# Performance work log

Hardware: AMD Instinct MI355X
Metric: run time of the kernel (lower is better)

## Reference

```python
import jax, jax.numpy as jnp
import numpy as np

N_HEADS = 16
D_EMBED = 1024
HEAD_DIM = D_EMBED // N_HEADS


def setup_inputs() -> dict:
    key = jax.random.key(0)
    ks = jax.random.split(key, 9)
    s = 1.0 / np.sqrt(D_EMBED)
    def lin(kw, kb):
        W = jax.random.uniform(kw, (D_EMBED, D_EMBED), jnp.float32, -s, s)
        b = jax.random.uniform(kb, (D_EMBED,), jnp.float32, -s, s)
        return W, b
    q_w, q_b = lin(ks[0], ks[1])
    k_w, k_b = lin(ks[2], ks[3])
    v_w, v_b = lin(ks[4], ks[5])
    o_w, o_b = lin(ks[6], ks[7])
    x = jax.random.normal(ks[8], (4, 2048, D_EMBED), jnp.float32)
    return {"x": x, "q_w": q_w, "q_b": q_b, "k_w": k_w, "k_b": k_b,
            "v_w": v_w, "v_b": v_b, "o_w": o_w, "o_b": o_b}


def reference(x, q_w, q_b, k_w, k_b, v_w, v_b, o_w, o_b):
    B, S, _ = x.shape
    # projections; W stored as [in, out] so y = x @ W + b (matches nn.Linear math)
    def split_heads(y):
        return y.reshape(B, S, N_HEADS, HEAD_DIM).transpose(0, 2, 1, 3)  # [B,H,S,D]
    q = split_heads(x @ q_w + q_b)
    k = split_heads(x @ k_w + k_b)
    v = split_heads(x @ v_w + v_b)
    scale = 1.0 / np.sqrt(HEAD_DIM).astype(np.float32)
    scores = jnp.einsum('bhqd,bhkd->bhqk', q, k) * scale  # [B,H,S,S]
    weights = jax.nn.softmax(scores, axis=-1)
    attn = jnp.einsum('bhqk,bhkd->bhqd', weights, v)  # [B,H,S,D]
    attn = attn.transpose(0, 2, 1, 3).reshape(B, S, D_EMBED)
    return attn @ o_w + o_b
```

## Files before the change

### kernel.cpp

```cpp
#include <hip/hip_runtime.h>
#include <hip/hip_bf16.h>
#include <math.h>

typedef __attribute__((ext_vector_type(8))) short bf16x8;
typedef __attribute__((ext_vector_type(4))) float f32x4;

#define D_EMBED 1024
#define SEQ 2048
#define NH 16
#define HD 64
#define QSCALE 0.1803368801111204f

__device__ __forceinline__ short f2bf(float f) {
    union { float f; unsigned u; } v; v.f = f;
    return (short)((v.u + 0x7FFFu + ((v.u >> 16) & 1u)) >> 16);
}

__device__ __forceinline__ unsigned pk_bf16(float a, float b) {
#if __has_builtin(__builtin_amdgcn_cvt_pk_bf16_f32)
    typedef __attribute__((ext_vector_type(2))) __bf16 vbf2;
    union { vbf2 v; unsigned u; } c;
    c.v = __builtin_amdgcn_cvt_pk_bf16_f32(a, b);
    return c.u;
#else
    return (unsigned)(unsigned short)f2bf(a) | ((unsigned)(unsigned short)f2bf(b) << 16);
#endif
}

__device__ __forceinline__ float exp2f_(float x) {
#if __has_builtin(__builtin_amdgcn_exp2f)
    return __builtin_amdgcn_exp2f(x);
#else
    return __expf(x * 0.6931471805599453f);
#endif
}

typedef __attribute__((address_space(1))) const void gvoid_t;
typedef __attribute__((address_space(3))) void lvoid_t;
__device__ __forceinline__ void glds16(const void* g, void* l) {
    __builtin_amdgcn_global_load_lds((gvoid_t*)g, (lvoid_t*)l, 16, 0, 0);
}

__global__ __launch_bounds__(256) void xconv_kernel(const float* __restrict__ x,
                                                    short* __restrict__ xb)
{
    size_t i = ((size_t)blockIdx.x * 256 + threadIdx.x) * 8;
    float4 f0 = *(const float4*)(x + i);
    float4 f1 = *(const float4*)(x + i + 4);
    uint4 o;
    o.x = pk_bf16(f0.x, f0.y); o.y = pk_bf16(f0.z, f0.w);
    o.z = pk_bf16(f1.x, f1.y); o.w = pk_bf16(f1.z, f1.w);
    *(uint4*)(xb + i) = o;
}

__global__ __launch_bounds__(256) void wtrans_kernel(
    const float* __restrict__ w0, const float* __restrict__ w1,
    const float* __restrict__ w2, const float* __restrict__ w3,
    short* __restrict__ wt)
{
    __shared__ float tile[64][65];
    const float* W = (blockIdx.z == 0) ? w0 : (blockIdx.z == 1) ? w1
                   : (blockIdx.z == 2) ? w2 : w3;
    short* out = wt + (size_t)blockIdx.z * D_EMBED * D_EMBED;
    int k0 = blockIdx.x * 64, n0 = blockIdx.y * 64;
    #pragma unroll
    for (int i = 0; i < 16; i++) {
        int idx = threadIdx.x + i * 256; int r = idx >> 6, c = idx & 63;
        tile[r][c] = W[(size_t)(k0 + r) * D_EMBED + n0 + c];
    }
    __syncthreads();
    #pragma unroll
    for (int i = 0; i < 16; i++) {
        int idx = threadIdx.x + i * 256; int r = idx >> 6, c = idx & 63;
        out[(size_t)(n0 + r) * D_EMBED + k0 + c] = f2bf(tile[c][r]);
    }
}

__global__ __launch_bounds__(256) void gemm_qkv_kernel(
    const short* __restrict__ xb, const short* __restrict__ wt,
    const float* __restrict__ qb, const float* __restrict__ kb, const float* __restrict__ vb,
    short* __restrict__ qo, short* __restrict__ ko, short* __restrict__ vto)
{
    __shared__ __attribute__((aligned(16))) short As[128][32];
    __shared__ __attribute__((aligned(16))) short Bs[128][32];
    const int tid = threadIdx.x;
    const int lane = tid & 63, wv = tid >> 6;
    const int l16 = lane & 15, quad = lane >> 4;
    const int wm = (wv & 1) * 64, wn = (wv >> 1) * 64;
    const int m0 = blockIdx.y * 128, n0 = blockIdx.x * 128;

    const short* aptr0 = xb + (size_t)(m0 + (tid >> 2)) * D_EMBED + (tid & 3) * 8;
    const short* aptr1 = aptr0 + (size_t)64 * D_EMBED;
    const short* bptr0 = wt + (size_t)(n0 + (tid >> 2)) * D_EMBED + (tid & 3) * 8;
    const short* bptr1 = bptr0 + (size_t)64 * D_EMBED;
    char* aldsb = (char*)&As[0][0] + wv * 1024;
    char* bldsb = (char*)&Bs[0][0] + wv * 1024;

    f32x4 acc[4][4];
    #pragma unroll
    for (int a = 0; a < 4; a++)
        #pragma unroll
        for (int b = 0; b < 4; b++) acc[a][b] = (f32x4){0.f, 0.f, 0.f, 0.f};

    for (int k0 = 0; k0 < D_EMBED; k0 += 32) {
        __syncthreads();
        glds16(aptr0 + k0, aldsb);
        glds16(aptr1 + k0, aldsb + 4096);
        glds16(bptr0 + k0, bldsb);
        glds16(bptr1 + k0, bldsb + 4096);
        __syncthreads();
        bf16x8 af[4], bfr[4];
        #pragma unroll
        for (int mi = 0; mi < 4; mi++) af[mi]  = *(const bf16x8*)&As[wm + mi * 16 + l16][quad * 8];
        #pragma unroll
        for (int ni = 0; ni < 4; ni++) bfr[ni] = *(const bf16x8*)&Bs[wn + ni * 16 + l16][quad * 8];
        #pragma unroll
        for (int mi = 0; mi < 4; mi++)
            #pragma unroll
            for (int ni = 0; ni < 4; ni++)
                acc[mi][ni] = __builtin_amdgcn_mfma_f32_16x16x32_bf16(af[mi], bfr[ni], acc[mi][ni], 0, 0, 0);
    }

    const int zz = n0 >> 10;
    const int ncol0 = (n0 & 1023) + wn;
    const float* bias = (zz == 0) ? qb : (zz == 1) ? kb : vb;
    #pragma unroll
    for (int mi = 0; mi < 4; mi++)
        #pragma unroll
        for (int ni = 0; ni < 4; ni++)
            #pragma unroll
            for (int rg = 0; rg < 4; rg++) {
                int row = m0 + wm + mi * 16 + quad * 4 + rg;
                int col = ncol0 + ni * 16 + l16;
                float v = acc[mi][ni][rg] + bias[col];
                int b = row >> 11, s = row & 2047, h = col >> 6, d = col & 63;
                if (zz == 0)      qo[(((size_t)(b * NH + h)) * SEQ + s) * HD + d] = f2bf(v * QSCALE);
                else if (zz == 1) ko[(((size_t)(b * NH + h)) * SEQ + s) * HD + d] = f2bf(v);
                else              vto[(((size_t)(b * NH + h)) * HD + d) * SEQ + s] = f2bf(v);
            }
}

__global__ __launch_bounds__(256) void flash_kernel(
    const short* __restrict__ Q, const short* __restrict__ K,
    const short* __restrict__ Vt, short* __restrict__ attn)
{
    __shared__ __attribute__((aligned(16))) short Ks[64][64];
    __shared__ __attribute__((aligned(16))) short Vs[64][64];
    __shared__ __attribute__((aligned(16))) short Ps[4][64][72];
    const int bh = blockIdx.y, qt = blockIdx.x;
    const int tid = threadIdx.x, lane = tid & 63, wv = tid >> 6;
    const int l16 = lane & 15, quad = lane >> 4;
    const int sw = l16 & 7;

    bf16x8 qf[4][2];
    #pragma unroll
    for (int g = 0; g < 4; g++) {
        const short* qp = Q + ((size_t)bh * SEQ + qt * 256 + wv * 64 + g * 16 + l16) * HD;
        qf[g][0] = *(const bf16x8*)(qp + quad * 8);
        qf[g][1] = *(const bf16x8*)(qp + 32 + quad * 8);
    }

    const int sr = tid >> 3;
    const int scg = (tid & 7) ^ (sr & 7);
    const short* kp0 = K  + ((size_t)bh * SEQ + sr) * HD + scg * 8;
    const short* vp0 = Vt + ((size_t)bh * HD + sr) * SEQ + scg * 8;
    char* kldsb = (char*)&Ks[0][0] + wv * 1024;
    char* vldsb = (char*)&Vs[0][0] + wv * 1024;

    float lsum[4] = {0.f, 0.f, 0.f, 0.f};
    f32x4 oacc[4][4];
    #pragma unroll
    for (int g = 0; g < 4; g++)
        #pragma unroll
        for (int di = 0; di < 4; di++) oacc[g][di] = (f32x4){0.f, 0.f, 0.f, 0.f};

    for (int kt = 0; kt < SEQ; kt += 64) {
        __syncthreads();
        glds16(kp0 + (size_t)kt * HD, kldsb);
        glds16(kp0 + (size_t)(kt + 32) * HD, kldsb + 4096);
        glds16(vp0 + kt, vldsb);
        glds16(vp0 + (size_t)32 * SEQ + kt, vldsb + 4096);
        __syncthreads();

        bf16x8 kf[4][2];
        #pragma unroll
        for (int ni = 0; ni < 4; ni++) {
            kf[ni][0] = *(const bf16x8*)&Ks[ni * 16 + l16][((quad    ) ^ sw) * 8];
            kf[ni][1] = *(const bf16x8*)&Ks[ni * 16 + l16][((quad + 4) ^ sw) * 8];
        }

        #pragma unroll
        for (int g = 0; g < 4; g++) {
            f32x4 sacc[4];
            #pragma unroll
            for (int ni = 0; ni < 4; ni++) {
                sacc[ni] = (f32x4){0.f, 0.f, 0.f, 0.f};
                sacc[ni] = __builtin_amdgcn_mfma_f32_16x16x32_bf16(kf[ni][0], qf[g][0], sacc[ni], 0, 0, 0);
                sacc[ni] = __builtin_amdgcn_mfma_f32_16x16x32_bf16(kf[ni][1], qf[g][1], sacc[ni], 0, 0, 0);
            }
            short* prow = &Ps[wv][g * 16 + l16][0];
            float ps = 0.f;
            #pragma unroll
            for (int ni = 0; ni < 4; ni++) {
                float p0 = exp2f_(sacc[ni][0]);
                float p1 = exp2f_(sacc[ni][1]);
                float p2 = exp2f_(sacc[ni][2]);
                float p3 = exp2f_(sacc[ni][3]);
                ps += (p0 + p1) + (p2 + p3);
                uint2 pw; pw.x = pk_bf16(p0, p1); pw.y = pk_bf16(p2, p3);
                *(uint2*)(prow + ni * 16 + quad * 4) = pw;
            }
            lsum[g] += ps;
        }

        bf16x8 vf[4][2];
        #pragma unroll
        for (int di = 0; di < 4; di++) {
            vf[di][0] = *(const bf16x8*)&Vs[di * 16 + l16][((quad    ) ^ sw) * 8];
            vf[di][1] = *(const bf16x8*)&Vs[di * 16 + l16][((quad + 4) ^ sw) * 8];
        }
        #pragma unroll
        for (int g = 0; g < 4; g++) {
            const short* prow = &Ps[wv][g * 16 + l16][0];
            bf16x8 pf0 = *(const bf16x8*)(prow + quad * 8);
            bf16x8 pf1 = *(const bf16x8*)(prow + 32 + quad * 8);
            #pragma unroll
            for (int di = 0; di < 4; di++) {
                oacc[g][di] = __builtin_amdgcn_mfma_f32_16x16x32_bf16(pf0, vf[di][0], oacc[g][di], 0, 0, 0);
                oacc[g][di] = __builtin_amdgcn_mfma_f32_16x16x32_bf16(pf1, vf[di][1], oacc[g][di], 0, 0, 0);
            }
        }
    }

    const int b = bh >> 4, h = bh & 15;
    #pragma unroll
    for (int g = 0; g < 4; g++) {
        float l = lsum[g];
        l += __shfl_xor(l, 16);
        l += __shfl_xor(l, 32);
        float rl[4];
        #pragma unroll
        for (int rg = 0; rg < 4; rg++) rl[rg] = 1.0f / __shfl(l, quad * 4 + rg);
        #pragma unroll
        for (int di = 0; di < 4; di++)
            #pragma unroll
            for (int rg = 0; rg < 4; rg++) {
                int s = qt * 256 + wv * 64 + g * 16 + quad * 4 + rg;
                int col = h * HD + di * 16 + l16;
                attn[((size_t)b * SEQ + s) * D_EMBED + col] = f2bf(oacc[g][di][rg] * rl[rg]);
            }
    }
}

__global__ __launch_bounds__(256) void gemm_out_kernel(
    const short* __restrict__ attn, const short* __restrict__ wt_o,
    const float* __restrict__ ob, float* __restrict__ out)
{
    __shared__ __attribute__((aligned(16))) short As[128][32];
    __shared__ __attribute__((aligned(16))) short Bs[128][32];
    const int tid = threadIdx.x;
    const int lane = tid & 63, wv = tid >> 6;
    const int l16 = lane & 15, quad = lane >> 4;
    const int wm = (wv & 1) * 64, wn = (wv >> 1) * 64;
    const int m0 = blockIdx.y * 128, n0 = blockIdx.x * 128;

    const short* aptr0 = attn + (size_t)(m0 + (tid >> 2)) * D_EMBED + (tid & 3) * 8;
    const short* aptr1 = aptr0 + (size_t)64 * D_EMBED;
    const short* bptr0 = wt_o + (size_t)(n0 + (tid >> 2)) * D_EMBED + (tid & 3) * 8;
    const short* bptr1 = bptr0 + (size_t)64 * D_EMBED;
    char* aldsb = (char*)&As[0][0] + wv * 1024;
    char* bldsb = (char*)&Bs[0][0] + wv * 1024;

    f32x4 acc[4][4];
    #pragma unroll
    for (int a = 0; a < 4; a++)
        #pragma unroll
        for (int b = 0; b < 4; b++) acc[a][b] = (f32x4){0.f, 0.f, 0.f, 0.f};

    for (int k0 = 0; k0 < D_EMBED; k0 += 32) {
        __syncthreads();
        glds16(aptr0 + k0, aldsb);
        glds16(aptr1 + k0, aldsb + 4096);
        glds16(bptr0 + k0, bldsb);
        glds16(bptr1 + k0, bldsb + 4096);
        __syncthreads();
        bf16x8 af[4], bfr[4];
        #pragma unroll
        for (int mi = 0; mi < 4; mi++) af[mi]  = *(const bf16x8*)&As[wm + mi * 16 + l16][quad * 8];
        #pragma unroll
        for (int ni = 0; ni < 4; ni++) bfr[ni] = *(const bf16x8*)&Bs[wn + ni * 16 + l16][quad * 8];
        #pragma unroll
        for (int mi = 0; mi < 4; mi++)
            #pragma unroll
            for (int ni = 0; ni < 4; ni++)
                acc[mi][ni] = __builtin_amdgcn_mfma_f32_16x16x32_bf16(af[mi], bfr[ni], acc[mi][ni], 0, 0, 0);
    }

    #pragma unroll
    for (int mi = 0; mi < 4; mi++)
        #pragma unroll
        for (int ni = 0; ni < 4; ni++)
            #pragma unroll
            for (int rg = 0; rg < 4; rg++) {
                int row = m0 + wm + mi * 16 + quad * 4 + rg;
                int col = n0 + wn + ni * 16 + l16;
                out[(size_t)row * D_EMBED + col] = acc[mi][ni][rg] + ob[col];
            }
}

extern "C" void kernel_launch(void* const* d_in, const int* in_sizes, int n_in,
                              void* d_out, int out_size, void* d_ws, size_t ws_size,
                              hipStream_t stream) {
    const float* x  = (const float*)d_in[0];
    const float* qw = (const float*)d_in[1];
    const float* qb = (const float*)d_in[2];
    const float* kw = (const float*)d_in[3];
    const float* kb = (const float*)d_in[4];
    const float* vw = (const float*)d_in[5];
    const float* vb = (const float*)d_in[6];
    const float* ow = (const float*)d_in[7];
    const float* ob = (const float*)d_in[8];

    char* ws = (char*)d_ws;
    short* xb  = (short*)(ws);
    short* wt  = (short*)(ws + (size_t)(16 << 20));
    short* q   = (short*)(ws + (size_t)(24 << 20));
    short* k   = (short*)(ws + (size_t)(40 << 20));
    short* vt  = (short*)(ws + (size_t)(56 << 20));
    short* at  = xb;

    xconv_kernel<<<4096, 256, 0, stream>>>(x, xb);
    wtrans_kernel<<<dim3(16, 16, 4), 256, 0, stream>>>(qw, kw, vw, ow, wt);
    gemm_qkv_kernel<<<dim3(24, 64), 256, 0, stream>>>(xb, wt, qb, kb, vb, q, k, vt);
    flash_kernel<<<dim3(8, 64), 256, 0, stream>>>(q, k, vt, at);
    gemm_out_kernel<<<dim3(8, 64), 256, 0, stream>>>(at, wt + (size_t)3 * D_EMBED * D_EMBED, ob, (float*)d_out);
}
```

Before: 327.4 us.

## Merge prep kernels, stage V transpose via LDS, load K directly, shrink out-GEMM tile

Folds the x conversion and the weight transpose into one launch, saving a kernel launch. The V-projection epilogue now transposes through shared memory so V^T is written with coalesced 16-byte stores instead of scattered 2-byte stores. The flash kernel reads K fragments straight from global memory (relying on cache) instead of staging them in LDS, and moves one barrier later so the score computation can overlap the V load. The output GEMM uses 128x64 tiles, doubling its block count for better CU occupancy, at the cost of lower per-block data reuse.

Result: faster. 319.0 us (-2.6%).

```diff
diff --git a/kernel.cpp b/kernel.cpp
--- a/kernel.cpp
+++ b/kernel.cpp
@@ -41,38 +41,38 @@
     __builtin_amdgcn_global_load_lds((gvoid_t*)g, (lvoid_t*)l, 16, 0, 0);
 }
 
-__global__ __launch_bounds__(256) void xconv_kernel(const float* __restrict__ x,
-                                                    short* __restrict__ xb)
-{
-    size_t i = ((size_t)blockIdx.x * 256 + threadIdx.x) * 8;
-    float4 f0 = *(const float4*)(x + i);
-    float4 f1 = *(const float4*)(x + i + 4);
-    uint4 o;
-    o.x = pk_bf16(f0.x, f0.y); o.y = pk_bf16(f0.z, f0.w);
-    o.z = pk_bf16(f1.x, f1.y); o.w = pk_bf16(f1.z, f1.w);
-    *(uint4*)(xb + i) = o;
-}
-
-__global__ __launch_bounds__(256) void wtrans_kernel(
+__global__ __launch_bounds__(256) void prep_kernel(
+    const float* __restrict__ x,
     const float* __restrict__ w0, const float* __restrict__ w1,
     const float* __restrict__ w2, const float* __restrict__ w3,
-    short* __restrict__ wt)
+    short* __restrict__ wt, short* __restrict__ xb)
 {
     __shared__ float tile[64][65];
-    const float* W = (blockIdx.z == 0) ? w0 : (blockIdx.z == 1) ? w1
-                   : (blockIdx.z == 2) ? w2 : w3;
-    short* out = wt + (size_t)blockIdx.z * D_EMBED * D_EMBED;
-    int k0 = blockIdx.x * 64, n0 = blockIdx.y * 64;
-    #pragma unroll
-    for (int i = 0; i < 16; i++) {
-        int idx = threadIdx.x + i * 256; int r = idx >> 6, c = idx & 63;
-        tile[r][c] = W[(size_t)(k0 + r) * D_EMBED + n0 + c];
-    }
-    __syncthreads();
-    #pragma unroll
-    for (int i = 0; i < 16; i++) {
-        int idx = threadIdx.x + i * 256; int r = idx >> 6, c = idx & 63;
-        out[(size_t)(n0 + r) * D_EMBED + k0 + c] = f2bf(tile[c][r]);
+    const int bid = blockIdx.x;
+    if (bid < 1024) {
+        const int z = bid >> 8, rem = bid & 255;
+        const float* W = (z == 0) ? w0 : (z == 1) ? w1 : (z == 2) ? w2 : w3;
+        short* out = wt + (size_t)z * D_EMBED * D_EMBED;
+        int k0 = (rem & 15) * 64, n0 = (rem >> 4) * 64;
+        #pragma unroll
+        for (int i = 0; i < 16; i++) {
+            int idx = threadIdx.x + i * 256; int r = idx >> 6, c = idx & 63;
+            tile[r][c] = W[(size_t)(k0 + r) * D_EMBED + n0 + c];
+        }
+        __syncthreads();
+        #pragma unroll
+        for (int i = 0; i < 16; i++) {
+            int idx = threadIdx.x + i * 256; int r = idx >> 6, c = idx & 63;
+            out[(size_t)(n0 + r) * D_EMBED + k0 + c] = f2bf(tile[c][r]);
+        }
+    } else {
+        size_t i = ((size_t)(bid - 1024) * 256 + threadIdx.x) * 8;
+        float4 f0 = *(const float4*)(x + i);
+        float4 f1 = *(const float4*)(x + i + 4);
+        uint4 o;
+        o.x = pk_bf16(f0.x, f0.y); o.y = pk_bf16(f0.z, f0.w);
+        o.z = pk_bf16(f1.x, f1.y); o.w = pk_bf16(f1.z, f1.w);
+        *(uint4*)(xb + i) = o;
     }
 }
 
@@ -81,8 +81,10 @@
     const float* __restrict__ qb, const float* __restrict__ kb, const float* __restrict__ vb,
     short* __restrict__ qo, short* __restrict__ ko, short* __restrict__ vto)
 {
-    __shared__ __attribute__((aligned(16))) short As[128][32];
-    __shared__ __attribute__((aligned(16))) short Bs[128][32];
+    __shared__ __attribute__((aligned(16))) union ShQKV {
+        struct { short As[128][32]; short Bs[128][32]; } ab;
+        short Es[64][136];
+    } sh;
     const int tid = threadIdx.x;
     const int lane = tid & 63, wv = tid >> 6;
     const int l16 = lane & 15, quad = lane >> 4;
@@ -93,8 +95,8 @@
     const short* aptr1 = aptr0 + (size_t)64 * D_EMBED;
     const short* bptr0 = wt + (size_t)(n0 + (tid >> 2)) * D_EMBED + (tid & 3) * 8;
     const short* bptr1 = bptr0 + (size_t)64 * D_EMBED;
-    char* aldsb = (char*)&As[0][0] + wv * 1024;
-    char* bldsb = (char*)&Bs[0][0] + wv * 1024;
+    char* aldsb = (char*)&sh.ab.As[0][0] + wv * 1024;
+    char* bldsb = (char*)&sh.ab.Bs[0][0] + wv * 1024;
 
     f32x4 acc[4][4];
     #pragma unroll
@@ -111,9 +113,9 @@
         __syncthreads();
         bf16x8 af[4], bfr[4];
         #pragma unroll
-        for (int mi = 0; mi < 4; mi++) af[mi]  = *(const bf16x8*)&As[wm + mi * 16 + l16][quad * 8];
-        #pragma unroll
-        for (int ni = 0; ni < 4; ni++) bfr[ni] = *(const bf16x8*)&Bs[wn + ni * 16 + l16][quad * 8];
+        for (int mi = 0; mi < 4; mi++) af[mi]  = *(const bf16x8*)&sh.ab.As[wm + mi * 16 + l16][quad * 8];
+        #pragma unroll
+        for (int ni = 0; ni < 4; ni++) bfr[ni] = *(const bf16x8*)&sh.ab.Bs[wn + ni * 16 + l16][quad * 8];
         #pragma unroll
         for (int mi = 0; mi < 4; mi++)
             #pragma unroll
@@ -122,29 +124,60 @@
     }
 
     const int zz = n0 >> 10;
-    const int ncol0 = (n0 & 1023) + wn;
-    const float* bias = (zz == 0) ? qb : (zz == 1) ? kb : vb;
-    #pragma unroll
-    for (int mi = 0; mi < 4; mi++)
-        #pragma unroll
-        for (int ni = 0; ni < 4; ni++)
-            #pragma unroll
-            for (int rg = 0; rg < 4; rg++) {
-                int row = m0 + wm + mi * 16 + quad * 4 + rg;
-                int col = ncol0 + ni * 16 + l16;
-                float v = acc[mi][ni][rg] + bias[col];
-                int b = row >> 11, s = row & 2047, h = col >> 6, d = col & 63;
-                if (zz == 0)      qo[(((size_t)(b * NH + h)) * SEQ + s) * HD + d] = f2bf(v * QSCALE);
-                else if (zz == 1) ko[(((size_t)(b * NH + h)) * SEQ + s) * HD + d] = f2bf(v);
-                else              vto[(((size_t)(b * NH + h)) * HD + d) * SEQ + s] = f2bf(v);
-            }
+    if (zz == 2) {
+        const int b = m0 >> 11, st0 = m0 & 2047;
+        const int hbase = (n0 & 1023) >> 6;
+        #pragma unroll
+        for (int h2 = 0; h2 < 2; h2++) {
+            __syncthreads();
+            if ((wv >> 1) == h2) {
+                #pragma unroll
+                for (int mi = 0; mi < 4; mi++) {
+                    int sbase = (wv & 1) * 64 + mi * 16 + quad * 4;
+                    #pragma unroll
+                    for (int ni = 0; ni < 4; ni++) {
+                        int d = ni * 16 + l16;
+                        float bv = vb[(n0 & 1023) + h2 * 64 + d];
+                        uint2 pw;
+                        pw.x = pk_bf16(acc[mi][ni][0] + bv, acc[mi][ni][1] + bv);
+                        pw.y = pk_bf16(acc[mi][ni][2] + bv, acc[mi][ni][3] + bv);
+                        *(uint2*)&sh.Es[d][sbase] = pw;
+                    }
+                }
+            }
+            __syncthreads();
+            const int h = hbase + h2;
+            #pragma unroll
+            for (int j = 0; j < 4; j++) {
+                int d = j * 16 + (tid >> 4);
+                int sc = (tid & 15) * 8;
+                bf16x8 vv = *(const bf16x8*)&sh.Es[d][sc];
+                *(bf16x8*)(vto + ((size_t)(b * NH + h) * HD + d) * SEQ + st0 + sc) = vv;
+            }
+        }
+    } else {
+        const int ncol0 = (n0 & 1023) + wn;
+        const float* bias = (zz == 0) ? qb : kb;
+        #pragma unroll
+        for (int mi = 0; mi < 4; mi++)
+            #pragma unroll
+            for (int ni = 0; ni < 4; ni++)
+                #pragma unroll
+                for (int rg = 0; rg < 4; rg++) {
+                    int row = m0 + wm + mi * 16 + quad * 4 + rg;
+                    int col = ncol0 + ni * 16 + l16;
+                    float v = acc[mi][ni][rg] + bias[col];
+                    int b = row >> 11, s = row & 2047, h = col >> 6, d = col & 63;
+                    if (zz == 0) qo[(((size_t)(b * NH + h)) * SEQ + s) * HD + d] = f2bf(v * QSCALE);
+                    else         ko[(((size_t)(b * NH + h)) * SEQ + s) * HD + d] = f2bf(v);
+                }
+    }
 }
 
 __global__ __launch_bounds__(256) void flash_kernel(
     const short* __restrict__ Q, const short* __restrict__ K,
     const short* __restrict__ Vt, short* __restrict__ attn)
 {
-    __shared__ __attribute__((aligned(16))) short Ks[64][64];
     __shared__ __attribute__((aligned(16))) short Vs[64][64];
     __shared__ __attribute__((aligned(16))) short Ps[4][64][72];
     const int bh = blockIdx.y, qt = blockIdx.x;
@@ -162,10 +195,10 @@
 
     const int sr = tid >> 3;
     const int scg = (tid & 7) ^ (sr & 7);
-    const short* kp0 = K  + ((size_t)bh * SEQ + sr) * HD + scg * 8;
     const short* vp0 = Vt + ((size_t)bh * HD + sr) * SEQ + scg * 8;
-    char* kldsb = (char*)&Ks[0][0] + wv * 1024;
     char* vldsb = (char*)&Vs[0][0] + wv * 1024;
+
+    const short* kb0 = K + ((size_t)bh * SEQ + l16) * HD + quad * 8;
 
     float lsum[4] = {0.f, 0.f, 0.f, 0.f};
     f32x4 oacc[4][4];
@@ -176,17 +209,15 @@
 
     for (int kt = 0; kt < SEQ; kt += 64) {
         __syncthreads();
-        glds16(kp0 + (size_t)kt * HD, kldsb);
-        glds16(kp0 + (size_t)(kt + 32) * HD, kldsb + 4096);
         glds16(vp0 + kt, vldsb);
         glds16(vp0 + (size_t)32 * SEQ + kt, vldsb + 4096);
-        __syncthreads();
 
         bf16x8 kf[4][2];
         #pragma unroll
         for (int ni = 0; ni < 4; ni++) {
-            kf[ni][0] = *(const bf16x8*)&Ks[ni * 16 + l16][((quad    ) ^ sw) * 8];
-            kf[ni][1] = *(const bf16x8*)&Ks[ni * 16 + l16][((quad + 4) ^ sw) * 8];
+            const short* kp = kb0 + (size_t)(kt + ni * 16) * HD;
+            kf[ni][0] = *(const bf16x8*)kp;
+            kf[ni][1] = *(const bf16x8*)(kp + 32);
         }
 
         #pragma unroll
@@ -213,6 +244,8 @@
             lsum[g] += ps;
         }
 
+        __syncthreads();
+
         bf16x8 vf[4][2];
         #pragma unroll
         for (int di = 0; di < 4; di++) {
@@ -257,49 +290,47 @@
     const float* __restrict__ ob, float* __restrict__ out)
 {
     __shared__ __attribute__((aligned(16))) short As[128][32];
-    __shared__ __attribute__((aligned(16))) short Bs[128][32];
+    __shared__ __attribute__((aligned(16))) short Bs[64][32];
     const int tid = threadIdx.x;
     const int lane = tid & 63, wv = tid >> 6;
     const int l16 = lane & 15, quad = lane >> 4;
-    const int wm = (wv & 1) * 64, wn = (wv >> 1) * 64;
-    const int m0 = blockIdx.y * 128, n0 = blockIdx.x * 128;
+    const int wm = (wv & 1) * 64, wn = (wv >> 1) * 32;
+    const int m0 = blockIdx.y * 128, n0 = blockIdx.x * 64;
 
     const short* aptr0 = attn + (size_t)(m0 + (tid >> 2)) * D_EMBED + (tid & 3) * 8;
     const short* aptr1 = aptr0 + (size_t)64 * D_EMBED;
     const short* bptr0 = wt_o + (size_t)(n0 + (tid >> 2)) * D_EMBED + (tid & 3) * 8;
-    const short* bptr1 = bptr0 + (size_t)64 * D_EMBED;
     char* aldsb = (char*)&As[0][0] + wv * 1024;
     char* bldsb = (char*)&Bs[0][0] + wv * 1024;
 
-    f32x4 acc[4][4];
+    f32x4 acc[4][2];
     #pragma unroll
     for (int a = 0; a < 4; a++)
         #pragma unroll
-        for (int b = 0; b < 4; b++) acc[a][b] = (f32x4){0.f, 0.f, 0.f, 0.f};
+        for (int b = 0; b < 2; b++) acc[a][b] = (f32x4){0.f, 0.f, 0.f, 0.f};
 
     for (int k0 = 0; k0 < D_EMBED; k0 += 32) {
         __syncthreads();
         glds16(aptr0 + k0, aldsb);
         glds16(aptr1 + k0, aldsb + 4096);
         glds16(bptr0 + k0, bldsb);
-        glds16(bptr1 + k0, bldsb + 4096);
-        __syncthreads();
-        bf16x8 af[4], bfr[4];
+        __syncthreads();
+        bf16x8 af[4], bfr[2];
         #pragma unroll
         for (int mi = 0; mi < 4; mi++) af[mi]  = *(const bf16x8*)&As[wm + mi * 16 + l16][quad * 8];
         #pragma unroll
-        for (int ni = 0; ni < 4; ni++) bfr[ni] = *(const bf16x8*)&Bs[wn + ni * 16 + l16][quad * 8];
+        for (int ni = 0; ni < 2; ni++) bfr[ni] = *(const bf16x8*)&Bs[wn + ni * 16 + l16][quad * 8];
         #pragma unroll
         for (int mi = 0; mi < 4; mi++)
             #pragma unroll
-            for (int ni = 0; ni < 4; ni++)
+            for (int ni = 0; ni < 2; ni++)
                 acc[mi][ni] = __builtin_amdgcn_mfma_f32_16x16x32_bf16(af[mi], bfr[ni], acc[mi][ni], 0, 0, 0);
     }
 
     #pragma unroll
     for (int mi = 0; mi < 4; mi++)
         #pragma unroll
-        for (int ni = 0; ni < 4; ni++)
+        for (int ni = 0; ni < 2; ni++)
             #pragma unroll
             for (int rg = 0; rg < 4; rg++) {
                 int row = m0 + wm + mi * 16 + quad * 4 + rg;
@@ -329,9 +360,8 @@
     short* vt  = (short*)(ws + (size_t)(56 << 20));
     short* at  = xb;
 
-    xconv_kernel<<<4096, 256, 0, stream>>>(x, xb);
-    wtrans_kernel<<<dim3(16, 16, 4), 256, 0, stream>>>(qw, kw, vw, ow, wt);
+    prep_kernel<<<5120, 256, 0, stream>>>(x, qw, kw, vw, ow, wt, xb);
     gemm_qkv_kernel<<<dim3(24, 64), 256, 0, stream>>>(xb, wt, qb, kb, vb, q, k, vt);
     flash_kernel<<<dim3(8, 64), 256, 0, stream>>>(q, k, vt, at);
-    gemm_out_kernel<<<dim3(8, 64), 256, 0, stream>>>(at, wt + (size_t)3 * D_EMBED * D_EMBED, ob, (float*)d_out);
-}
+    gemm_out_kernel<<<dim3(16, 64), 256, 0, stream>>>(at, wt + (size_t)3 * D_EMBED * D_EMBED, ob, (float*)d_out);
+}
```
